# Optimization experiments

Hardware: AMD Instinct MI355X
Metric: run time of the kernel (lower is better)

## Reference

```python
import jax, jax.numpy as jnp
import numpy as np

NEG = -1e30  # finite stand-in for -inf so logaddexp grads stay NaN-free


def setup_inputs() -> dict:
    key = jax.random.key(0)
    k1, k2 = jax.random.split(key)
    B, T, V, L = 32, 1024, 1024, 100
    logits = jax.random.normal(k1, (B, T, V), dtype=jnp.float32)
    # labels exclude the blank symbol (blank = V-1)
    targets = jax.random.randint(k2, (B, L), 0, V - 1, dtype=jnp.int32)
    return {"targets": targets, "logits": logits}


def reference(targets, logits):
    # tf.nn.ctc_loss(targets, logits, L, T, logits_time_major=False, blank_index=-1)
    # followed by reduce_mean. Standard CTC forward algorithm in log space.
    B, T, V = logits.shape
    L = targets.shape[1]
    S = 2 * L + 1
    blank = V - 1

    logp = jax.nn.log_softmax(logits, axis=-1)  # [B,T,V]

    # extended label sequence: blank, l1, blank, l2, ..., blank  -> [B,S]
    ext = jnp.full((B, S), blank, dtype=targets.dtype).at[:, 1::2].set(targets)
    # skip transition s-2 -> s allowed iff ext[s] != blank and ext[s] != ext[s-2]
    allow_skip = jnp.pad((ext[:, 2:] != blank) & (ext[:, 2:] != ext[:, :-2]),
                         ((0, 0), (2, 0)))  # [B,S]

    # gather per-step log-probs of extended labels: [B,T,S] -> [T,B,S]
    lp_ext = jnp.take_along_axis(logp, ext[:, None, :], axis=2)
    lp_ext = jnp.transpose(lp_ext, (1, 0, 2))

    alpha0 = (jnp.full((B, S), NEG, dtype=logp.dtype)
              .at[:, 0].set(lp_ext[0, :, 0])
              .at[:, 1].set(lp_ext[0, :, 1]))

    def step(alpha, lp_t):
        a1 = jnp.pad(alpha[:, :-1], ((0, 0), (1, 0)), constant_values=NEG)
        a2 = jnp.where(allow_skip,
                       jnp.pad(alpha[:, :-2], ((0, 0), (2, 0)), constant_values=NEG),
                       NEG)
        alpha_new = jnp.logaddexp(jnp.logaddexp(alpha, a1), a2) + lp_t
        return alpha_new, None

    alphaT, _ = jax.lax.scan(step, alpha0, lp_ext[1:])
    per_example_loss = -jnp.logaddexp(alphaT[:, -1], alphaT[:, -2])  # [B]
    return jnp.mean(per_example_loss)
```

## Files before the change

### kernel.cpp

```cpp
#include <hip/hip_runtime.h>
#include <math.h>

#define DEV static __device__ __forceinline__

constexpr int Bn = 32, Tn = 1024, Vn = 1024, Ln = 100, Sn = 2 * Ln + 1;
constexpr int   RW   = 208;
constexpr float LN2F = 0.6931471805599453f;
constexpr int   TILE = 32;

DEV float dpp_up1_f(float v) {
    return __builtin_bit_cast(float,
        __builtin_amdgcn_update_dpp(0, __builtin_bit_cast(int, v), 0x138, 0xf, 0xf, false));
}
DEV int dpp_up1_i(int v) {
    return __builtin_amdgcn_update_dpp(v, v, 0x138, 0xf, 0xf, false);
}

DEV float wave_max(float m) {
    #pragma unroll
    for (int off = 32; off; off >>= 1) m = fmaxf(m, __shfl_xor(m, off));
    return m;
}
DEV float wave_sum(float s) {
    #pragma unroll
    for (int off = 32; off; off >>= 1) s += __shfl_xor(s, off);
    return s;
}

__global__ __launch_bounds__(256) void pre_kernel(const int* __restrict__ targets,
                                                  const float* __restrict__ logits,
                                                  float* __restrict__ lp_ext) {
    __shared__ float rows[2][Vn];
    __shared__ float red[2][8];
    const int t    = threadIdx.x;
    const int lane = t & 63;
    const int wid  = t >> 6;
    const int r0   = blockIdx.x * 2;
    const int b    = r0 >> 10;

    float4 v0 = ((const float4*)(logits + (size_t)r0 * Vn))[t];
    float4 v1 = ((const float4*)(logits + (size_t)(r0 + 1) * Vn))[t];
    ((float4*)rows[0])[t] = v0;
    ((float4*)rows[1])[t] = v1;

    float m0 = fmaxf(fmaxf(v0.x, v0.y), fmaxf(v0.z, v0.w));
    float m1 = fmaxf(fmaxf(v1.x, v1.y), fmaxf(v1.z, v1.w));
    m0 = wave_max(m0); m1 = wave_max(m1);
    if (lane == 0) { red[0][wid] = m0; red[1][wid] = m1; }
    __syncthreads();
    m0 = fmaxf(fmaxf(red[0][0], red[0][1]), fmaxf(red[0][2], red[0][3]));
    m1 = fmaxf(fmaxf(red[1][0], red[1][1]), fmaxf(red[1][2], red[1][3]));

    float e0 = __expf(v0.x - m0) + __expf(v0.y - m0) + __expf(v0.z - m0) + __expf(v0.w - m0);
    float e1 = __expf(v1.x - m1) + __expf(v1.y - m1) + __expf(v1.z - m1) + __expf(v1.w - m1);
    e0 = wave_sum(e0); e1 = wave_sum(e1);
    if (lane == 0) { red[0][4 + wid] = e0; red[1][4 + wid] = e1; }
    __syncthreads();
    const float lse0 = m0 + __logf((red[0][4] + red[0][5]) + (red[0][6] + red[0][7]));
    const float lse1 = m1 + __logf((red[1][4] + red[1][5]) + (red[1][6] + red[1][7]));

    if (t < RW) {
        int ei = ((t & 1) && t < Sn) ? targets[b * Ln + (t >> 1)] : (Vn - 1);
        lp_ext[(size_t)r0 * RW + t]       = __expf(rows[0][ei] - lse0);
        lp_ext[(size_t)(r0 + 1) * RW + t] = __expf(rows[1][ei] - lse1);
    }
}

__global__ __launch_bounds__(64, 1) void ctc_kernel(const int* __restrict__ targets,
                                                    const float* __restrict__ lp_ext,
                                                    float* __restrict__ loss) {
    const int b    = blockIdx.x;
    const int lane = threadIdx.x;

    float sk1f = 0.f, sk3f = 0.f;
    {
        const int* tg = targets + b * Ln;
        int s1 = 4 * lane + 1, s3 = 4 * lane + 3;
        if (s1 >= 3 && s1 < Sn) sk1f = (tg[s1 >> 1] != tg[(s1 - 3) >> 1]) ? 1.f : 0.f;
        if (s3 >= 3 && s3 < Sn) sk3f = (tg[s3 >> 1] != tg[(s3 - 3) >> 1]) ? 1.f : 0.f;
    }

    const float4* gb = (const float4*)(lp_ext + (size_t)b * Tn * RW);
    const int ll = (lane < 52) ? lane : 51;

    float4 bufA[TILE], bufB[TILE];
    #pragma unroll
    for (int u = 0; u < TILE; u++) bufA[u] = gb[(size_t)u * 52 + ll];
    #pragma unroll
    for (int u = 0; u < TILE; u++) bufB[u] = gb[(size_t)(TILE + u) * 52 + ll];

    float m0 = (lane == 0) ? 1.0f : 0.0f, m1 = 0.f, m2 = 0.f, m3 = 0.f;
    int   E  = 0;
    int   dE = 0;

    auto consume = [&](float4 (&pr)[TILE]) {
        #pragma unroll
        for (int u = 0; u < TILE; u++) {
            const float4 p = pr[u];
            float pmm = dpp_up1_f(m3);
            float pm1 = __builtin_amdgcn_ldexpf(pmm, dE);
            float n0 = (m0 + pm1) * p.x;
            float n1 = fmaf(pm1, sk1f, m0 + m1) * p.y;
            float n2 = (m2 + m1) * p.z;
            float n3 = fmaf(m1, sk3f, m2 + m3) * p.w;
            m0 = n0; m1 = n1; m2 = n2; m3 = n3;
            if ((u & 3) == 3) {
                float mx = fmaxf(fmaxf(m0, m1), fmaxf(m2, m3));
                int k = __builtin_amdgcn_frexp_expf(mx);
                int Enb_old = dpp_up1_i(E);
                E = (mx > 0.f) ? (E + k) : Enb_old;
                m0 = __builtin_amdgcn_ldexpf(m0, -k);
                m1 = __builtin_amdgcn_ldexpf(m1, -k);
                m2 = __builtin_amdgcn_ldexpf(m2, -k);
                m3 = __builtin_amdgcn_ldexpf(m3, -k);
                dE = dpp_up1_i(E) - E;
            }
        }
    };

    const int nt = Tn / TILE;
    for (int tb = 0; tb < nt; tb += 2) {
        consume(bufA);
        if (tb + 2 < nt) {
            #pragma unroll
            for (int u = 0; u < TILE; u++)
                bufA[u] = gb[(size_t)((tb + 2) * TILE + u) * 52 + ll];
        }
        consume(bufB);
        if (tb + 3 < nt) {
            #pragma unroll
            for (int u = 0; u < TILE; u++)
                bufB[u] = gb[(size_t)((tb + 3) * TILE + u) * 52 + ll];
        }
    }

    float q200 = __shfl(m0, 50); int E50 = __shfl(E, 50);
    float q199 = __shfl(m3, 49); int E49 = __shfl(E, 49);
    if (lane == 0) {
        float s = q200 + __builtin_amdgcn_ldexpf(q199, E49 - E50);
        loss[b] = -LN2F * ((float)E50 + __log2f(s));
    }
}

__global__ __launch_bounds__(64) void mean_kernel(const float* __restrict__ loss,
                                                  float* __restrict__ out) {
    int lane = threadIdx.x;
    float v = (lane < Bn) ? loss[lane] : 0.f;
    #pragma unroll
    for (int off = 32; off; off >>= 1) v += __shfl_xor(v, off);
    if (lane == 0) out[0] = v * (1.0f / Bn);
}

extern "C" void kernel_launch(void* const* d_in, const int* in_sizes, int n_in,
                              void* d_out, int out_size, void* d_ws, size_t ws_size,
                              hipStream_t stream) {
    const int*   targets = (const int*)d_in[0];
    const float* logits  = (const float*)d_in[1];

    float* lp_ext = (float*)d_ws;
    float* loss   = (float*)((char*)d_ws + (size_t)Bn * Tn * RW * sizeof(float) + 4096);

    pre_kernel<<<Bn * Tn / 2, 256, 0, stream>>>(targets, logits, lp_ext);
    ctc_kernel<<<Bn, 64, 0, stream>>>(targets, lp_ext, loss);
    mean_kernel<<<1, 64, 0, stream>>>(loss, (float*)d_out);
}
```

Before: 251.0 us.

## Compact lp_ext to unique labels plus one blank, fuse mean into CTC kernel

The intermediate per-timestep table now stores only the 100 label probabilities plus a single blank value (row width 104 instead of 208), roughly halving the intermediate write and read traffic. The CTC recurrence reads a float2 of label probabilities per lane plus a broadcast blank value. The separate mean kernel is removed: the last CTC block, found with an atomic ticket, does the final reduction, which saves one launch. The cost is an atomic counter and an extra scalar load per timestep.

```diff
diff --git a/kernel.cpp b/kernel.cpp
--- a/kernel.cpp
+++ b/kernel.cpp
@@ -4,7 +4,7 @@
 #define DEV static __device__ __forceinline__
 
 constexpr int Bn = 32, Tn = 1024, Vn = 1024, Ln = 100, Sn = 2 * Ln + 1;
-constexpr int   RW   = 208;
+constexpr int   PK   = 104;
 constexpr float LN2F = 0.6931471805599453f;
 constexpr int   TILE = 32;
 
@@ -29,7 +29,8 @@
 
 __global__ __launch_bounds__(256) void pre_kernel(const int* __restrict__ targets,
                                                   const float* __restrict__ logits,
-                                                  float* __restrict__ lp_ext) {
+                                                  float* __restrict__ lp_ext,
+                                                  int* __restrict__ cnt) {
     __shared__ float rows[2][Vn];
     __shared__ float red[2][8];
     const int t    = threadIdx.x;
@@ -38,6 +39,8 @@
     const int r0   = blockIdx.x * 2;
     const int b    = r0 >> 10;
 
+    if (blockIdx.x == 0 && t == 0) cnt[0] = 0;
+
     float4 v0 = ((const float4*)(logits + (size_t)r0 * Vn))[t];
     float4 v1 = ((const float4*)(logits + (size_t)(r0 + 1) * Vn))[t];
     ((float4*)rows[0])[t] = v0;
@@ -59,16 +62,28 @@
     const float lse0 = m0 + __logf((red[0][4] + red[0][5]) + (red[0][6] + red[0][7]));
     const float lse1 = m1 + __logf((red[1][4] + red[1][5]) + (red[1][6] + red[1][7]));
 
-    if (t < RW) {
-        int ei = ((t & 1) && t < Sn) ? targets[b * Ln + (t >> 1)] : (Vn - 1);
-        lp_ext[(size_t)r0 * RW + t]       = __expf(rows[0][ei] - lse0);
-        lp_ext[(size_t)(r0 + 1) * RW + t] = __expf(rows[1][ei] - lse1);
+    if (t < PK) {
+        float w0, w1;
+        if (t < 100) {
+            int ei = targets[b * Ln + t];
+            w0 = __expf(rows[0][ei] - lse0);
+            w1 = __expf(rows[1][ei] - lse1);
+        } else if (t == 100) {
+            w0 = __expf(rows[0][Vn - 1] - lse0);
+            w1 = __expf(rows[1][Vn - 1] - lse1);
+        } else {
+            w0 = 0.f; w1 = 0.f;
+        }
+        lp_ext[(size_t)r0 * PK + t]       = w0;
+        lp_ext[(size_t)(r0 + 1) * PK + t] = w1;
     }
 }
 
 __global__ __launch_bounds__(64, 1) void ctc_kernel(const int* __restrict__ targets,
                                                     const float* __restrict__ lp_ext,
-                                                    float* __restrict__ loss) {
+                                                    float* __restrict__ loss,
+                                                    int* __restrict__ cnt,
+                                                    float* __restrict__ out) {
     const int b    = blockIdx.x;
     const int lane = threadIdx.x;
 
@@ -80,29 +95,39 @@
         if (s3 >= 3 && s3 < Sn) sk3f = (tg[s3 >> 1] != tg[(s3 - 3) >> 1]) ? 1.f : 0.f;
     }
 
-    const float4* gb = (const float4*)(lp_ext + (size_t)b * Tn * RW);
-    const int ll = (lane < 52) ? lane : 51;
-
-    float4 bufA[TILE], bufB[TILE];
-    #pragma unroll
-    for (int u = 0; u < TILE; u++) bufA[u] = gb[(size_t)u * 52 + ll];
-    #pragma unroll
-    for (int u = 0; u < TILE; u++) bufB[u] = gb[(size_t)(TILE + u) * 52 + ll];
+    const float* gb = lp_ext + (size_t)b * Tn * PK;
+    const int ll = (lane < 51) ? lane : 51;
+
+    float2 lA[TILE], lB[TILE];
+    float  bA[TILE], bB[TILE];
+    #pragma unroll
+    for (int u = 0; u < TILE; u++) {
+        const float* row = gb + (size_t)u * PK;
+        lA[u] = ((const float2*)row)[ll];
+        bA[u] = row[100];
+    }
+    #pragma unroll
+    for (int u = 0; u < TILE; u++) {
+        const float* row = gb + (size_t)(TILE + u) * PK;
+        lB[u] = ((const float2*)row)[ll];
+        bB[u] = row[100];
+    }
 
     float m0 = (lane == 0) ? 1.0f : 0.0f, m1 = 0.f, m2 = 0.f, m3 = 0.f;
     int   E  = 0;
     int   dE = 0;
 
-    auto consume = [&](float4 (&pr)[TILE]) {
+    auto consume = [&](float2 (&lb)[TILE], float (&bb)[TILE]) {
         #pragma unroll
         for (int u = 0; u < TILE; u++) {
-            const float4 p = pr[u];
+            const float2 lp = lb[u];
+            const float  bl = bb[u];
             float pmm = dpp_up1_f(m3);
             float pm1 = __builtin_amdgcn_ldexpf(pmm, dE);
-            float n0 = (m0 + pm1) * p.x;
-            float n1 = fmaf(pm1, sk1f, m0 + m1) * p.y;
-            float n2 = (m2 + m1) * p.z;
-            float n3 = fmaf(m1, sk3f, m2 + m3) * p.w;
+            float n0 = (m0 + pm1) * bl;
+            float n1 = fmaf(pm1, sk1f, m0 + m1) * lp.x;
+            float n2 = (m2 + m1) * bl;
+            float n3 = fmaf(m1, sk3f, m2 + m3) * lp.y;
             m0 = n0; m1 = n1; m2 = n2; m3 = n3;
             if ((u & 3) == 3) {
                 float mx = fmaxf(fmaxf(m0, m1), fmaxf(m2, m3));
@@ -120,17 +145,23 @@
 
     const int nt = Tn / TILE;
     for (int tb = 0; tb < nt; tb += 2) {
-        consume(bufA);
+        consume(lA, bA);
         if (tb + 2 < nt) {
             #pragma unroll
-            for (int u = 0; u < TILE; u++)
-                bufA[u] = gb[(size_t)((tb + 2) * TILE + u) * 52 + ll];
-        }
-        consume(bufB);
+            for (int u = 0; u < TILE; u++) {
+                const float* row = gb + (size_t)((tb + 2) * TILE + u) * PK;
+                lA[u] = ((const float2*)row)[ll];
+                bA[u] = row[100];
+            }
+        }
+        consume(lB, bB);
         if (tb + 3 < nt) {
             #pragma unroll
-            for (int u = 0; u < TILE; u++)
-                bufB[u] = gb[(size_t)((tb + 3) * TILE + u) * 52 + ll];
+            for (int u = 0; u < TILE; u++) {
+                const float* row = gb + (size_t)((tb + 3) * TILE + u) * PK;
+                lB[u] = ((const float2*)row)[ll];
+                bB[u] = row[100];
+            }
         }
     }
 
@@ -140,15 +171,18 @@
         float s = q200 + __builtin_amdgcn_ldexpf(q199, E49 - E50);
         loss[b] = -LN2F * ((float)E50 + __log2f(s));
     }
-}
-
-__global__ __launch_bounds__(64) void mean_kernel(const float* __restrict__ loss,
-                                                  float* __restrict__ out) {
-    int lane = threadIdx.x;
-    float v = (lane < Bn) ? loss[lane] : 0.f;
-    #pragma unroll
-    for (int off = 32; off; off >>= 1) v += __shfl_xor(v, off);
-    if (lane == 0) out[0] = v * (1.0f / Bn);
+
+    __threadfence();
+    int ticket = 0;
+    if (lane == 0) ticket = atomicAdd(cnt, 1);
+    ticket = __shfl(ticket, 0);
+    if (ticket == Bn - 1) {
+        __threadfence();
+        float v = (lane < Bn) ? ((volatile const float*)loss)[lane] : 0.f;
+        #pragma unroll
+        for (int off = 32; off; off >>= 1) v += __shfl_xor(v, off);
+        if (lane == 0) out[0] = v * (1.0f / Bn);
+    }
 }
 
 extern "C" void kernel_launch(void* const* d_in, const int* in_sizes, int n_in,
@@ -158,9 +192,10 @@
     const float* logits  = (const float*)d_in[1];
 
     float* lp_ext = (float*)d_ws;
-    float* loss   = (float*)((char*)d_ws + (size_t)Bn * Tn * RW * sizeof(float) + 4096);
-
-    pre_kernel<<<Bn * Tn / 2, 256, 0, stream>>>(targets, logits, lp_ext);
-    ctc_kernel<<<Bn, 64, 0, stream>>>(targets, lp_ext, loss);
-    mean_kernel<<<1, 64, 0, stream>>>(loss, (float*)d_out);
-}
+    char*  tail   = (char*)d_ws + (size_t)Bn * Tn * PK * sizeof(float) + 4096;
+    float* loss   = (float*)tail;
+    int*   cnt    = (int*)(tail + 256);
+
+    pre_kernel<<<Bn * Tn / 2, 256, 0, stream>>>(targets, logits, lp_ext, cnt);
+    ctc_kernel<<<Bn, 64, 0, stream>>>(targets, lp_ext, loss, cnt, (float*)d_out);
+}
```

New measurement: 237.9 us. -5.2%, faster.
